# Kernel optimization log

Hardware: AMD Instinct MI355X
Metric: run time of the kernel (lower is better)

Reference implementation:

```python
import jax, jax.numpy as jnp
import numpy as np

N_NODES = 50000
N_EDGES = 800000
HIDDEN = 128
MLP_DIM = 64

def setup_inputs() -> dict:
    key = jax.random.key(0)
    k1, k2, k3, k4 = jax.random.split(key, 4)
    node_emb = jax.random.normal(k1, (N_NODES, HIDDEN), dtype=jnp.float32)
    edge_index = jax.random.randint(k2, (2, N_EDGES), 0, N_NODES, dtype=jnp.int64)
    # Xavier-uniform init like the torch module
    lim1 = float(np.sqrt(6.0 / (2 * HIDDEN + MLP_DIM)))
    lim2 = float(np.sqrt(6.0 / (MLP_DIM + 1)))
    W1 = jax.random.uniform(k3, (2 * HIDDEN, MLP_DIM), minval=-lim1, maxval=lim1, dtype=jnp.float32)
    b1 = jnp.zeros((MLP_DIM,), dtype=jnp.float32)
    W2 = jax.random.uniform(k4, (MLP_DIM, 1), minval=-lim2, maxval=lim2, dtype=jnp.float32)
    b2 = jnp.zeros((1,), dtype=jnp.float32)
    return {"node_emb": node_emb, "edge_index": edge_index, "W1": W1, "b1": b1, "W2": W2, "b2": b2}

def reference(node_emb, edge_index, W1, b1, W2, b2):
    src, dst = edge_index[0], edge_index[1]
    emb_src = node_emb[src]                      # [E, H] gather
    emb_dst = node_emb[dst]                      # [E, H] gather
    edge_emb = jnp.concatenate([emb_src, emb_dst], axis=1)  # [E, 2H]
    h = jax.nn.relu(edge_emb @ W1 + b1)          # [E, MLP_DIM]
    edge_logits = h @ W2 + b2                    # [E, 1]
    return edge_logits
```

## Files before the change

### kernel.cpp

```cpp
#include <hip/hip_runtime.h>
#include <hip/hip_bf16.h>


#define HIDDEN 128

typedef __attribute__((ext_vector_type(8))) short bf16x8;
typedef __attribute__((ext_vector_type(8))) unsigned short ushort8;
typedef __attribute__((ext_vector_type(4))) float f32x4;
typedef __attribute__((ext_vector_type(4))) int int4v;

#define AS_GLOBAL __attribute__((address_space(1)))
#define AS_LDS    __attribute__((address_space(3)))

__device__ inline unsigned short f32_to_bf16(float f) {
    unsigned int u = __float_as_uint(f);
    unsigned int r = (u + 0x7fffu + ((u >> 16) & 1u)) >> 16;
    return (unsigned short)r;
}

__global__ __launch_bounds__(256) void build_wt_scales(
    const float* __restrict__ W1,
    const float* __restrict__ b1,
    const float* __restrict__ W2,
    unsigned short* __restrict__ Wt,
    float* __restrict__ invs,
    float* __restrict__ w2s)
{
    if (blockIdx.x < 8) {
        const int gid = blockIdx.x * 256 + threadIdx.x;
        const int j  = gid >> 4;
        const int k0 = (gid & 15) * 8;
        const int rbase = k0 + ((j >= 64) ? 128 : 0);
        const int col = j & 63;
        ushort8 o;
        #pragma unroll
        for (int i = 0; i < 8; ++i)
            o[i] = f32_to_bf16(W1[(rbase + i) * 64 + col]);
        *(ushort8*)&Wt[j * 136 + k0] = o;
    } else {
        const int c = threadIdx.x;
        if (c < 64) {
            float sp = 0.f, sq = 0.f;
            for (int k = 0; k < 128; ++k) {
                float a = W1[k * 64 + c];
                float b = W1[(k + 128) * 64 + c];
                sp = fmaf(a, a, sp);
                sq = fmaf(b, b, sq);
            }
            float sig = sqrtf(fmaxf(sp, sq));
            float range = 4.8f * sig + fabsf(b1[c]);
            float inv = 127.f / range;
            invs[c] = inv;
            invs[c + 64] = inv;
            w2s[c] = W2[c] * (range / 127.f);
        }
    }
}

__global__ __launch_bounds__(256, 4) void precompute_pq_mfma(
    const float* __restrict__ node_emb,
    const unsigned short* __restrict__ Wt,
    const float* __restrict__ b1,
    const float* __restrict__ invs,
    char* __restrict__ PQ8,
    int n_nodes)
{
    __shared__ unsigned short Bt[128 * 136];

    const int t = threadIdx.x;
    const int wave = t >> 6, lane = t & 63;
    const int l15 = lane & 15;
    const int kq = (lane >> 4) * 8;
    const int m0 = blockIdx.x * 64;
    const int node = m0 + wave * 16 + l15;
    const bool valid = (node < n_nodes);

    {
        const char* gsrc = (const char*)Wt;
        char* ldst = (char*)Bt;
        #pragma unroll
        for (int it = 0; it < 8; ++it) {
            const int off = it * 4096 + wave * 1024;
            __builtin_amdgcn_global_load_lds(
                (const AS_GLOBAL void*)(gsrc + off + lane * 16),
                (AS_LDS void*)(ldst + off), 16, 0, 0);
        }
        if (wave < 2) {
            const int off = 32768 + wave * 1024;
            __builtin_amdgcn_global_load_lds(
                (const AS_GLOBAL void*)(gsrc + off + lane * 16),
                (AS_LDS void*)(ldst + off), 16, 0, 0);
        }
    }

    const float* arow = node_emb + (size_t)(valid ? node : 0) * HIDDEN + kq;
    float4 aLo[4], aHi[4];
    #pragma unroll
    for (int i = 0; i < 4; ++i) {
        if (valid) {
            aLo[i] = *(const float4*)(arow + i * 32);
            aHi[i] = *(const float4*)(arow + i * 32 + 4);
        } else {
            aLo[i] = make_float4(0.f, 0.f, 0.f, 0.f);
            aHi[i] = aLo[i];
        }
    }
    __syncthreads();

    f32x4 acc[8];
    #pragma unroll
    for (int c = 0; c < 8; ++c) acc[c] = (f32x4){0.f, 0.f, 0.f, 0.f};

    #pragma unroll
    for (int k0i = 0; k0i < 4; ++k0i) {
        union { bf16x8 v; __hip_bfloat162 h[4]; } ua;
        ua.h[0] = __float22bfloat162_rn(make_float2(aLo[k0i].x, aLo[k0i].y));
        ua.h[1] = __float22bfloat162_rn(make_float2(aLo[k0i].z, aLo[k0i].w));
        ua.h[2] = __float22bfloat162_rn(make_float2(aHi[k0i].x, aHi[k0i].y));
        ua.h[3] = __float22bfloat162_rn(make_float2(aHi[k0i].z, aHi[k0i].w));
        const int kbase = k0i * 32 + kq;
        #pragma unroll
        for (int c = 0; c < 8; ++c) {
            bf16x8 wf = *(const bf16x8*)&Bt[(c * 16 + l15) * 136 + kbase];
            acc[c] = __builtin_amdgcn_mfma_f32_16x16x32_bf16(wf, ua.v, acc[c], 0, 0, 0);
        }
    }

    if (valid) {
        const int rbase = (lane >> 4) * 4;
        float4 bias[4], isv[8];
        #pragma unroll
        for (int c = 0; c < 4; ++c) bias[c] = *(const float4*)&b1[c * 16 + rbase];
        #pragma unroll
        for (int c = 0; c < 8; ++c) isv[c] = *(const float4*)&invs[c * 16 + rbase];
        char* drow = PQ8 + (size_t)node * 128;
        #pragma unroll
        for (int c = 0; c < 8; ++c) {
            const float* bf = (const float*)&bias[c < 4 ? c : 0];
            const float* iv = (const float*)&isv[c];
            unsigned int pack = 0;
            #pragma unroll
            for (int reg = 0; reg < 4; ++reg) {
                float v = acc[c][reg] + ((c < 4) ? bf[reg] : 0.f);
                float qf = fminf(fmaxf(v * iv[reg], -127.f), 127.f);
                int qi = (int)rintf(qf);
                pack |= ((unsigned int)qi & 0xffu) << (8 * reg);
            }
            *(unsigned int*)&drow[c * 16 + rbase] = pack;
        }
    }
}

__global__ __launch_bounds__(256) void edge_mlp8(
    const char* __restrict__ PQ8,
    const int* __restrict__ edge_index,
    const float* __restrict__ w2s,
    const float* __restrict__ b2,
    float* __restrict__ out,
    int E)
{
    const int t = threadIdx.x;
    const int g = t & 3;
    const int slot = t >> 2;
    const int ebase = blockIdx.x * 256 + slot;

    float4 w[4];
    #pragma unroll
    for (int d = 0; d < 4; ++d) w[d] = *(const float4*)&w2s[g * 16 + d * 4];

    int src[4], dst[4];
    #pragma unroll
    for (int j = 0; j < 4; ++j) {
        src[j] = __builtin_nontemporal_load(&edge_index[ebase + 64 * j]);
        dst[j] = __builtin_nontemporal_load(&edge_index[E + ebase + 64 * j]);
    }

    int4v a[4], b[4];
    #pragma unroll
    for (int j = 0; j < 4; ++j) {
        a[j] = *(const int4v*)(PQ8 + (size_t)src[j] * 128 + g * 16);
        b[j] = *(const int4v*)(PQ8 + (size_t)dst[j] * 128 + 64 + g * 16);
    }

    float s[4] = {0.f, 0.f, 0.f, 0.f};
    #pragma unroll
    for (int j = 0; j < 4; ++j) {
        #pragma unroll
        for (int d = 0; d < 4; ++d) {
            const int av = a[j][d], bv = b[j][d];
            const float* wd = (const float*)&w[d];
            #pragma unroll
            for (int i = 0; i < 4; ++i) {
                int x = (int)(signed char)((unsigned int)av >> (8 * i))
                      + (int)(signed char)((unsigned int)bv >> (8 * i));
                x = (x > 0) ? x : 0;
                s[j] = fmaf((float)x, wd[i], s[j]);
            }
        }
    }

    #pragma unroll
    for (int j = 0; j < 4; ++j) {
        s[j] += __shfl_xor(s[j], 1, 64);
        s[j] += __shfl_xor(s[j], 2, 64);
    }

    if (g == 0) {
        const float bb = b2[0];
        #pragma unroll
        for (int j = 0; j < 4; ++j)
            __builtin_nontemporal_store(s[j] + bb, &out[ebase + 64 * j]);
    }
}

extern "C" void kernel_launch(void* const* d_in, const int* in_sizes, int n_in,
                              void* d_out, int out_size, void* d_ws, size_t ws_size,
                              hipStream_t stream) {
    const float* node_emb   = (const float*)d_in[0];
    const int*   edge_index = (const int*)d_in[1];
    const float* W1 = (const float*)d_in[2];
    const float* b1 = (const float*)d_in[3];
    const float* W2 = (const float*)d_in[4];
    const float* b2 = (const float*)d_in[5];
    float* out = (float*)d_out;

    const int n_nodes = in_sizes[0] / HIDDEN;
    const int E = in_sizes[1] / 2;

    char* PQ8 = (char*)d_ws;
    unsigned short* Wt = (unsigned short*)((char*)d_ws + (size_t)n_nodes * 128);
    float* invs = (float*)((char*)Wt + 128 * 136 * sizeof(unsigned short));
    float* w2s  = invs + 128;

    build_wt_scales<<<9, 256, 0, stream>>>(W1, b1, W2, Wt, invs, w2s);

    const int grid1 = (n_nodes + 63) / 64;
    precompute_pq_mfma<<<grid1, 256, 0, stream>>>(node_emb, Wt, b1, invs, PQ8, n_nodes);

    const int grid2 = E / 256;
    edge_mlp8<<<grid2, 256, 0, stream>>>(PQ8, edge_index, w2s, b2, out, E);
}
```

Before: 107.4 us.

## Fuse weight prep, node projection and edge MLP into one persistent kernel

Merges the three launches into a single persistent kernel of 1024 blocks. Each block rebuilds the transposed bf16 W1 tile and the quantisation scales in LDS, computes its node tile's int8 projections, then waits at an atomic grid-wide barrier before running a grid-stride loop over edge tiles. The aim is to remove two kernel launch gaps and the global round trips for Wt, invs and w2s. In exchange every block redundantly reads and transposes W1. The barrier depends on all 1024 blocks being co-resident, and its counter reset can race with blocks that see the flag left over from a previous call.

```diff
diff --git a/kernel.cpp b/kernel.cpp
--- a/kernel.cpp
+++ b/kernel.cpp
@@ -3,14 +3,11 @@
 
 
 #define HIDDEN 128
+#define GRID_BLOCKS 1024
 
 typedef __attribute__((ext_vector_type(8))) short bf16x8;
-typedef __attribute__((ext_vector_type(8))) unsigned short ushort8;
 typedef __attribute__((ext_vector_type(4))) float f32x4;
 typedef __attribute__((ext_vector_type(4))) int int4v;
-
-#define AS_GLOBAL __attribute__((address_space(1)))
-#define AS_LDS    __attribute__((address_space(3)))
 
 __device__ inline unsigned short f32_to_bf16(float f) {
     unsigned int u = __float_as_uint(f);
@@ -18,80 +15,40 @@
     return (unsigned short)r;
 }
 
-__global__ __launch_bounds__(256) void build_wt_scales(
+__global__ __launch_bounds__(256, 4) void fused_all(
+    const float* __restrict__ node_emb,
+    const int* __restrict__ edge_index,
     const float* __restrict__ W1,
     const float* __restrict__ b1,
     const float* __restrict__ W2,
-    unsigned short* __restrict__ Wt,
-    float* __restrict__ invs,
-    float* __restrict__ w2s)
-{
-    if (blockIdx.x < 8) {
-        const int gid = blockIdx.x * 256 + threadIdx.x;
-        const int j  = gid >> 4;
-        const int k0 = (gid & 15) * 8;
-        const int rbase = k0 + ((j >= 64) ? 128 : 0);
-        const int col = j & 63;
-        ushort8 o;
-        #pragma unroll
-        for (int i = 0; i < 8; ++i)
-            o[i] = f32_to_bf16(W1[(rbase + i) * 64 + col]);
-        *(ushort8*)&Wt[j * 136 + k0] = o;
-    } else {
-        const int c = threadIdx.x;
-        if (c < 64) {
-            float sp = 0.f, sq = 0.f;
-            for (int k = 0; k < 128; ++k) {
-                float a = W1[k * 64 + c];
-                float b = W1[(k + 128) * 64 + c];
-                sp = fmaf(a, a, sp);
-                sq = fmaf(b, b, sq);
-            }
-            float sig = sqrtf(fmaxf(sp, sq));
-            float range = 4.8f * sig + fabsf(b1[c]);
-            float inv = 127.f / range;
-            invs[c] = inv;
-            invs[c + 64] = inv;
-            w2s[c] = W2[c] * (range / 127.f);
-        }
-    }
-}
-
-__global__ __launch_bounds__(256, 4) void precompute_pq_mfma(
-    const float* __restrict__ node_emb,
-    const unsigned short* __restrict__ Wt,
-    const float* __restrict__ b1,
-    const float* __restrict__ invs,
+    const float* __restrict__ b2,
+    float* __restrict__ out,
     char* __restrict__ PQ8,
-    int n_nodes)
+    unsigned int* __restrict__ cnt,
+    unsigned int* __restrict__ flag,
+    int n_nodes, int E)
 {
     __shared__ unsigned short Bt[128 * 136];
+    __shared__ float nl[128];
+    __shared__ float invsL[128];
+    __shared__ float w2sL[64];
 
     const int t = threadIdx.x;
-    const int wave = t >> 6, lane = t & 63;
+    const int bid = blockIdx.x;
+    const unsigned int SENT = 0x5EBA11EDu;
+
+    if (bid == 0 && t == 0) {
+        __hip_atomic_store(cnt, 0u, __ATOMIC_RELAXED, __HIP_MEMORY_SCOPE_AGENT);
+        __hip_atomic_store(flag, SENT, __ATOMIC_RELEASE, __HIP_MEMORY_SCOPE_AGENT);
+    }
+
+    const int lane = t & 63;
     const int l15 = lane & 15;
     const int kq = (lane >> 4) * 8;
-    const int m0 = blockIdx.x * 64;
-    const int node = m0 + wave * 16 + l15;
-    const bool valid = (node < n_nodes);
-
-    {
-        const char* gsrc = (const char*)Wt;
-        char* ldst = (char*)Bt;
-        #pragma unroll
-        for (int it = 0; it < 8; ++it) {
-            const int off = it * 4096 + wave * 1024;
-            __builtin_amdgcn_global_load_lds(
-                (const AS_GLOBAL void*)(gsrc + off + lane * 16),
-                (AS_LDS void*)(ldst + off), 16, 0, 0);
-        }
-        if (wave < 2) {
-            const int off = 32768 + wave * 1024;
-            __builtin_amdgcn_global_load_lds(
-                (const AS_GLOBAL void*)(gsrc + off + lane * 16),
-                (AS_LDS void*)(ldst + off), 16, 0, 0);
-        }
-    }
+    const int n_tiles = (n_nodes + 63) >> 6;
+    const bool have = (bid < n_tiles);
+    const int node = bid * 64 + (t >> 6) * 16 + l15;
+    const bool valid = have && (node < n_nodes);
 
     const float* arow = node_emb + (size_t)(valid ? node : 0) * HIDDEN + kq;
     float4 aLo[4], aHi[4];
@@ -105,111 +62,154 @@
             aHi[i] = aLo[i];
         }
     }
-    __syncthreads();
+
+    #pragma unroll
+    for (int it = 0; it < 16; ++it) {
+        int slot = it * 256 + t;
+        int r = slot >> 4;
+        int c4 = (slot & 15) * 4;
+        float4 v = *(const float4*)&W1[r * 64 + c4];
+        int j = (r < 128) ? c4 : (c4 + 64);
+        int k = r & 127;
+        Bt[(j + 0) * 136 + k] = f32_to_bf16(v.x);
+        Bt[(j + 1) * 136 + k] = f32_to_bf16(v.y);
+        Bt[(j + 2) * 136 + k] = f32_to_bf16(v.z);
+        Bt[(j + 3) * 136 + k] = f32_to_bf16(v.w);
+    }
+    __syncthreads();
+
+    if (t < 128) {
+        float s = 0.f;
+        #pragma unroll
+        for (int i = 0; i < 16; ++i) {
+            bf16x8 vv = *(const bf16x8*)&Bt[t * 136 + i * 8];
+            #pragma unroll
+            for (int e = 0; e < 8; ++e) {
+                float f = __uint_as_float(((unsigned int)(unsigned short)vv[e]) << 16);
+                s = fmaf(f, f, s);
+            }
+        }
+        nl[t] = s;
+    }
 
     f32x4 acc[8];
     #pragma unroll
     for (int c = 0; c < 8; ++c) acc[c] = (f32x4){0.f, 0.f, 0.f, 0.f};
-
-    #pragma unroll
-    for (int k0i = 0; k0i < 4; ++k0i) {
-        union { bf16x8 v; __hip_bfloat162 h[4]; } ua;
-        ua.h[0] = __float22bfloat162_rn(make_float2(aLo[k0i].x, aLo[k0i].y));
-        ua.h[1] = __float22bfloat162_rn(make_float2(aLo[k0i].z, aLo[k0i].w));
-        ua.h[2] = __float22bfloat162_rn(make_float2(aHi[k0i].x, aHi[k0i].y));
-        ua.h[3] = __float22bfloat162_rn(make_float2(aHi[k0i].z, aHi[k0i].w));
-        const int kbase = k0i * 32 + kq;
-        #pragma unroll
-        for (int c = 0; c < 8; ++c) {
-            bf16x8 wf = *(const bf16x8*)&Bt[(c * 16 + l15) * 136 + kbase];
-            acc[c] = __builtin_amdgcn_mfma_f32_16x16x32_bf16(wf, ua.v, acc[c], 0, 0, 0);
-        }
-    }
+    if (have) {
+        #pragma unroll
+        for (int k0i = 0; k0i < 4; ++k0i) {
+            union { bf16x8 v; __hip_bfloat162 h[4]; } ua;
+            ua.h[0] = __float22bfloat162_rn(make_float2(aLo[k0i].x, aLo[k0i].y));
+            ua.h[1] = __float22bfloat162_rn(make_float2(aLo[k0i].z, aLo[k0i].w));
+            ua.h[2] = __float22bfloat162_rn(make_float2(aHi[k0i].x, aHi[k0i].y));
+            ua.h[3] = __float22bfloat162_rn(make_float2(aHi[k0i].z, aHi[k0i].w));
+            const int kbase = k0i * 32 + kq;
+            #pragma unroll
+            for (int c = 0; c < 8; ++c) {
+                bf16x8 wf = *(const bf16x8*)&Bt[(c * 16 + l15) * 136 + kbase];
+                acc[c] = __builtin_amdgcn_mfma_f32_16x16x32_bf16(wf, ua.v, acc[c], 0, 0, 0);
+            }
+        }
+    }
+    __syncthreads();
+
+    if (t < 64) {
+        float sig = sqrtf(fmaxf(nl[t], nl[t + 64]));
+        float range = 4.8f * sig + fabsf(b1[t]);
+        float inv = 127.f / range;
+        invsL[t] = inv;
+        invsL[t + 64] = inv;
+        w2sL[t] = W2[t] * (range / 127.f);
+    }
+    __syncthreads();
 
     if (valid) {
         const int rbase = (lane >> 4) * 4;
-        float4 bias[4], isv[8];
-        #pragma unroll
-        for (int c = 0; c < 4; ++c) bias[c] = *(const float4*)&b1[c * 16 + rbase];
-        #pragma unroll
-        for (int c = 0; c < 8; ++c) isv[c] = *(const float4*)&invs[c * 16 + rbase];
         char* drow = PQ8 + (size_t)node * 128;
         #pragma unroll
         for (int c = 0; c < 8; ++c) {
-            const float* bf = (const float*)&bias[c < 4 ? c : 0];
-            const float* iv = (const float*)&isv[c];
+            float4 iv = *(const float4*)&invsL[c * 16 + rbase];
+            float4 bf = (c < 4) ? *(const float4*)&b1[c * 16 + rbase]
+                                : make_float4(0.f, 0.f, 0.f, 0.f);
+            const float* ivp = (const float*)&iv;
+            const float* bfp = (const float*)&bf;
             unsigned int pack = 0;
             #pragma unroll
             for (int reg = 0; reg < 4; ++reg) {
-                float v = acc[c][reg] + ((c < 4) ? bf[reg] : 0.f);
-                float qf = fminf(fmaxf(v * iv[reg], -127.f), 127.f);
+                float v = acc[c][reg] + bfp[reg];
+                float qf = fminf(fmaxf(v * ivp[reg], -127.f), 127.f);
                 int qi = (int)rintf(qf);
                 pack |= ((unsigned int)qi & 0xffu) << (8 * reg);
             }
             *(unsigned int*)&drow[c * 16 + rbase] = pack;
         }
     }
-}
-
-__global__ __launch_bounds__(256) void edge_mlp8(
-    const char* __restrict__ PQ8,
-    const int* __restrict__ edge_index,
-    const float* __restrict__ w2s,
-    const float* __restrict__ b2,
-    float* __restrict__ out,
-    int E)
-{
-    const int t = threadIdx.x;
+
+    __threadfence();
+    if (t == 0) {
+        while (__hip_atomic_load(flag, __ATOMIC_ACQUIRE, __HIP_MEMORY_SCOPE_AGENT) != SENT)
+            __builtin_amdgcn_s_sleep(16);
+        __hip_atomic_fetch_add(cnt, 1u, __ATOMIC_ACQ_REL, __HIP_MEMORY_SCOPE_AGENT);
+        while (__hip_atomic_load(cnt, __ATOMIC_ACQUIRE, __HIP_MEMORY_SCOPE_AGENT)
+               < (unsigned int)GRID_BLOCKS)
+            __builtin_amdgcn_s_sleep(16);
+    }
+    __syncthreads();
+    __threadfence();
+
     const int g = t & 3;
     const int slot = t >> 2;
-    const int ebase = blockIdx.x * 256 + slot;
-
     float4 w[4];
     #pragma unroll
-    for (int d = 0; d < 4; ++d) w[d] = *(const float4*)&w2s[g * 16 + d * 4];
-
-    int src[4], dst[4];
-    #pragma unroll
-    for (int j = 0; j < 4; ++j) {
-        src[j] = __builtin_nontemporal_load(&edge_index[ebase + 64 * j]);
-        dst[j] = __builtin_nontemporal_load(&edge_index[E + ebase + 64 * j]);
-    }
-
-    int4v a[4], b[4];
-    #pragma unroll
-    for (int j = 0; j < 4; ++j) {
-        a[j] = *(const int4v*)(PQ8 + (size_t)src[j] * 128 + g * 16);
-        b[j] = *(const int4v*)(PQ8 + (size_t)dst[j] * 128 + 64 + g * 16);
-    }
-
-    float s[4] = {0.f, 0.f, 0.f, 0.f};
-    #pragma unroll
-    for (int j = 0; j < 4; ++j) {
-        #pragma unroll
-        for (int d = 0; d < 4; ++d) {
-            const int av = a[j][d], bv = b[j][d];
-            const float* wd = (const float*)&w[d];
-            #pragma unroll
-            for (int i = 0; i < 4; ++i) {
-                int x = (int)(signed char)((unsigned int)av >> (8 * i))
-                      + (int)(signed char)((unsigned int)bv >> (8 * i));
-                x = (x > 0) ? x : 0;
-                s[j] = fmaf((float)x, wd[i], s[j]);
-            }
-        }
-    }
-
-    #pragma unroll
-    for (int j = 0; j < 4; ++j) {
-        s[j] += __shfl_xor(s[j], 1, 64);
-        s[j] += __shfl_xor(s[j], 2, 64);
-    }
-
-    if (g == 0) {
-        const float bb = b2[0];
-        #pragma unroll
-        for (int j = 0; j < 4; ++j)
-            __builtin_nontemporal_store(s[j] + bb, &out[ebase + 64 * j]);
+    for (int d = 0; d < 4; ++d) w[d] = *(const float4*)&w2sL[g * 16 + d * 4];
+    const float bb = b2[0];
+    const int n_etiles = E >> 8;
+
+    for (int tile = bid; tile < n_etiles; tile += GRID_BLOCKS) {
+        const int ebase = tile * 256 + slot;
+
+        int src[4], dst[4];
+        #pragma unroll
+        for (int j = 0; j < 4; ++j) {
+            src[j] = __builtin_nontemporal_load(&edge_index[ebase + 64 * j]);
+            dst[j] = __builtin_nontemporal_load(&edge_index[E + ebase + 64 * j]);
+        }
+
+        int4v a[4], b[4];
+        #pragma unroll
+        for (int j = 0; j < 4; ++j) {
+            a[j] = *(const int4v*)(PQ8 + (size_t)src[j] * 128 + g * 16);
+            b[j] = *(const int4v*)(PQ8 + (size_t)dst[j] * 128 + 64 + g * 16);
+        }
+
+        float s[4] = {0.f, 0.f, 0.f, 0.f};
+        #pragma unroll
+        for (int j = 0; j < 4; ++j) {
+            #pragma unroll
+            for (int d = 0; d < 4; ++d) {
+                const int av = a[j][d], bv = b[j][d];
+                const float* wd = (const float*)&w[d];
+                #pragma unroll
+                for (int i = 0; i < 4; ++i) {
+                    int x = (int)(signed char)((unsigned int)av >> (8 * i))
+                          + (int)(signed char)((unsigned int)bv >> (8 * i));
+                    x = (x > 0) ? x : 0;
+                    s[j] = fmaf((float)x, wd[i], s[j]);
+                }
+            }
+        }
+
+        #pragma unroll
+        for (int j = 0; j < 4; ++j) {
+            s[j] += __shfl_xor(s[j], 1, 64);
+            s[j] += __shfl_xor(s[j], 2, 64);
+        }
+
+        if (g == 0) {
+            #pragma unroll
+            for (int j = 0; j < 4; ++j)
+                __builtin_nontemporal_store(s[j] + bb, &out[ebase + 64 * j]);
+        }
     }
 }
 
@@ -228,15 +228,10 @@
     const int E = in_sizes[1] / 2;
 
     char* PQ8 = (char*)d_ws;
-    unsigned short* Wt = (unsigned short*)((char*)d_ws + (size_t)n_nodes * 128);
-    float* invs = (float*)((char*)Wt + 128 * 136 * sizeof(unsigned short));
-    float* w2s  = invs + 128;
-
-    build_wt_scales<<<9, 256, 0, stream>>>(W1, b1, W2, Wt, invs, w2s);
-
-    const int grid1 = (n_nodes + 63) / 64;
-    precompute_pq_mfma<<<grid1, 256, 0, stream>>>(node_emb, Wt, b1, invs, PQ8, n_nodes);
-
-    const int grid2 = E / 256;
-    edge_mlp8<<<grid2, 256, 0, stream>>>(PQ8, edge_index, w2s, b2, out, E);
+    size_t pq_bytes = (size_t)n_nodes * 128;
+    unsigned int* cnt  = (unsigned int*)((char*)d_ws + pq_bytes);
+    unsigned int* flag = (unsigned int*)((char*)d_ws + pq_bytes + 128);
+
+    fused_all<<<GRID_BLOCKS, 256, 0, stream>>>(
+        node_emb, edge_index, W1, b1, W2, b2, out, PQ8, cnt, flag, n_nodes, E);
 }
```

Result: slower. 370.7 us (+245.1%).
